# Kernel optimization log

Hardware: AMD Instinct MI355X
Metric: run time of the kernel (lower is better)

Reference implementation:

```python
import jax, jax.numpy as jnp
import numpy as np

B, N, DEG = 4, 2048, 16
HID, NH = 768, 12
D = HID // NH
N_REL = 64
E = B * N * DEG


def setup_inputs() -> dict:
    key = jax.random.key(0)
    k_x, k_r, k_q, k_k, k_v, k_e = jax.random.split(key, 6)
    node_states = jax.random.normal(k_x, (B, N, HID), dtype=jnp.float32) * 0.02
    # Deterministically unique edges: each (b, i) attends to DEG distinct tails.
    b_idx = jnp.repeat(jnp.arange(B), N * DEG)
    i_idx = jnp.tile(jnp.repeat(jnp.arange(N), DEG), B)
    offs = jnp.tile(jnp.arange(1, DEG + 1), B * N)
    t_idx = (i_idx + offs) % N
    r_idx = jax.random.randint(k_r, (E,), 0, N_REL)
    edge_indices = jnp.stack([b_idx, i_idx, t_idx, r_idx]).astype(jnp.int32)
    # Linear params (torch: y = x @ W.T + b)
    Wq = jax.random.normal(k_q, (HID, HID), dtype=jnp.float32) * 0.02
    Wk = jax.random.normal(k_k, (HID, HID), dtype=jnp.float32) * 0.02
    Wv = jax.random.normal(k_v, (HID, HID), dtype=jnp.float32) * 0.02
    bq = jnp.zeros((HID,), jnp.float32)
    bk = jnp.zeros((HID,), jnp.float32)
    bv = jnp.zeros((HID,), jnp.float32)
    rel_emb = jax.random.normal(k_e, (N_REL, HID), dtype=jnp.float32) * 0.02
    rel_emb = rel_emb.at[0].set(0.0)  # TOKEN_TO_TOKEN_RELATION_ID zeroed
    return {"node_states": node_states, "edge_indices": edge_indices,
            "Wq": Wq, "bq": bq, "Wk": Wk, "bk": bk, "Wv": Wv, "bv": bv,
            "rel_emb": rel_emb}


def reference(node_states, edge_indices, Wq, bq, Wk, bk, Wv, bv, rel_emb):
    Bv, Nv, H = node_states.shape
    Q = node_states @ Wq.T + bq
    K = node_states @ Wk.T + bk
    V = node_states @ Wv.T + bv
    b, i, t, r = edge_indices[0], edge_indices[1], edge_indices[2], edge_indices[3]
    # Translated key: K[b, tail] - relation embedding
    k_shift = (K[b, t] - rel_emb[r]).reshape(-1, NH, D)  # (E, nh, d)
    q_e = Q[b, i].reshape(-1, NH, D)                      # (E, nh, d)
    scale = jnp.sqrt(jnp.asarray(D, node_states.dtype))
    logits = jnp.einsum('ehd,ehd->eh', q_e, k_shift) / scale  # (E, nh)
    # Sparse softmax over tail dim == segment softmax per (batch, head node)
    seg = b * Nv + i
    n_seg = Bv * Nv
    m = jax.ops.segment_max(logits, seg, num_segments=n_seg)
    ex = jnp.exp(logits - m[seg])
    den = jax.ops.segment_sum(ex, seg, num_segments=n_seg)
    probs = ex / den[seg]  # (E, nh); dropout is identity in eval
    # Aggregate: out[b, i] += probs * V[b, t]
    Vt = V.reshape(Bv, Nv, NH, D)
    contrib = probs[:, :, None] * Vt[b, t]  # (E, nh, d)
    out = jax.ops.segment_sum(contrib, seg, num_segments=n_seg)
    return out.reshape(Bv, Nv, H)
```

## Files before the change

### kernel.cpp

```cpp
#include <hip/hip_runtime.h>

#define B_    4
#define N_    2048
#define HID_  768
#define NH_   12
#define E_    131072
#define M_    8192
#define NREL_ 64
#define G_    16
#define BAND_ 32
#define VP_   40
#define PP_   40

typedef unsigned short u16;
typedef unsigned int   u32;
typedef short bf16x8 __attribute__((ext_vector_type(8)));
typedef float f32x4  __attribute__((ext_vector_type(4)));

__device__ __forceinline__ u16 f2bf(float x) {
  u32 u = __float_as_uint(x);
  u += 0x7fffu + ((u >> 16) & 1u);
  return (u16)(u >> 16);
}
__device__ __forceinline__ float bflo(u32 u) { return __uint_as_float(u << 16); }
__device__ __forceinline__ float bfhi(u32 u) { return __uint_as_float(u & 0xffff0000u); }
__device__ __forceinline__ float bf1(u16 v) { return __uint_as_float(((u32)v) << 16); }

__device__ __forceinline__ void load_lds16(const u16* g, u16* l) {
  __builtin_amdgcn_global_load_lds((__attribute__((address_space(1))) void*)(g),
                                   (__attribute__((address_space(3))) void*)(l),
                                   16, 0, 0);
}

__global__ __launch_bounds__(256) void k_convert(
    const float4* __restrict__ X, const float4* __restrict__ Wq,
    const float4* __restrict__ Wk, const float4* __restrict__ Wv,
    const float4* __restrict__ rel,
    ushort4* __restrict__ Xbf, ushort4* __restrict__ Wbf, ushort4* __restrict__ Rbf) {
  const int NX4 = (M_ * HID_) / 4;
  const int NW4 = (HID_ * HID_) / 4;
  const int NR4 = (NREL_ * HID_) / 4;
  int tid = blockIdx.x * 256 + threadIdx.x;
  const float4* src; ushort4* dst; int off;
  if (tid < NX4) { src = X; dst = Xbf; off = tid; }
  else if (tid < NX4 + 3 * NW4) {
    int t2 = tid - NX4;
    int wi = t2 / NW4;
    off = t2 - wi * NW4;
    src = (wi == 0) ? Wq : (wi == 1) ? Wk : Wv;
    dst = Wbf + (size_t)wi * NW4;
  } else {
    off = tid - NX4 - 3 * NW4;
    if (off >= NR4) return;
    src = rel; dst = Rbf;
  }
  float4 v = src[off];
  ushort4 o;
  o.x = f2bf(v.x); o.y = f2bf(v.y); o.z = f2bf(v.z); o.w = f2bf(v.w);
  dst[off] = o;
}

__global__ __launch_bounds__(256, 3) void k_gemm(
    const u16* __restrict__ Xbf, const u16* __restrict__ Wbf,
    const float* __restrict__ bq, const float* __restrict__ bk, const float* __restrict__ bv,
    u16* __restrict__ Qb, u16* __restrict__ Kb, u16* __restrict__ Vb) {
  __shared__ u16 As[128 * 64];
  __shared__ u16 Bs[192 * 64];
  const int tid = threadIdx.x;
  const int w = tid >> 6, lane = tid & 63;
  const int m0 = blockIdx.x * 128;
  const int ny = blockIdx.y;
  const int widx = ny >> 2;
  const int nl0 = (ny & 3) * 192;
  const u16* Wp = Wbf + (size_t)widx * (HID_ * HID_);
  u16* Op = (widx == 0) ? Qb : (widx == 1) ? Kb : Vb;
  const float* bias = (widx == 0) ? bq : (widx == 1) ? bk : bv;

  f32x4 acc[4][6] = {};
  const int wm = w >> 1, wn = w & 1;
  const int lm = lane & 15, lg = lane >> 4;

  for (int kt = 0; kt < HID_ / 64; ++kt) {
    const int k0 = kt * 64;
    __syncthreads();
#pragma unroll
    for (int ii = 0; ii < 4; ++ii) {
      const int sb = (ii * 4 + w) * 64;
      const int s = sb + lane;
      const int m = s >> 3;
      const int g = (s & 7) ^ (m & 7);
      load_lds16(Xbf + (size_t)(m0 + m) * HID_ + k0 + g * 8, &As[sb * 8]);
    }
#pragma unroll
    for (int ii = 0; ii < 6; ++ii) {
      const int sb = (ii * 4 + w) * 64;
      const int s = sb + lane;
      const int m = s >> 3;
      const int g = (s & 7) ^ (m & 7);
      load_lds16(Wp + (size_t)(nl0 + m) * HID_ + k0 + g * 8, &Bs[sb * 8]);
    }
    __syncthreads();
#pragma unroll
    for (int kk = 0; kk < 2; ++kk) {
      bf16x8 af[4], bfr[6];
#pragma unroll
      for (int mt = 0; mt < 4; ++mt) {
        const int m = wm * 64 + mt * 16 + lm;
        const int g = (kk * 4 + lg) ^ (m & 7);
        af[mt] = *(const bf16x8*)&As[m * 64 + g * 8];
      }
#pragma unroll
      for (int nt = 0; nt < 6; ++nt) {
        const int n = wn * 96 + nt * 16 + lm;
        const int g = (kk * 4 + lg) ^ (n & 7);
        bfr[nt] = *(const bf16x8*)&Bs[n * 64 + g * 8];
      }
#pragma unroll
      for (int mt = 0; mt < 4; ++mt)
#pragma unroll
        for (int nt = 0; nt < 6; ++nt)
          acc[mt][nt] = __builtin_amdgcn_mfma_f32_16x16x32_bf16(af[mt], bfr[nt], acc[mt][nt], 0, 0, 0);
    }
  }
#pragma unroll
  for (int nt = 0; nt < 6; ++nt) {
    const int c = nl0 + wn * 96 + nt * 16 + lm;
    const float bb = bias[c];
#pragma unroll
    for (int mt = 0; mt < 4; ++mt) {
      const int rbase = m0 + wm * 64 + mt * 16 + lg * 4;
#pragma unroll
      for (int r = 0; r < 4; ++r)
        Op[(size_t)(rbase + r) * HID_ + c] = f2bf(acc[mt][nt][r] + bb);
    }
  }
}

__global__ __launch_bounds__(256) void k_qrel(
    const u16* __restrict__ Qb, const u16* __restrict__ Rbf, u16* __restrict__ QRelb) {
  const int tid = threadIdx.x, w = tid >> 6, lane = tid & 63;
  const int lm = lane & 15, quad = lane >> 4;
  const int m0 = blockIdx.x * 32 + (w & 1) * 16;
  const int h0 = (w >> 1) * 6;
#pragma unroll
  for (int hh = 0; hh < 6; ++hh) {
    const int h = h0 + hh;
    const u16* qp = Qb + (size_t)(m0 + lm) * HID_ + h * 64 + quad * 8;
    bf16x8 a0 = *(const bf16x8*)(qp);
    bf16x8 a1 = *(const bf16x8*)(qp + 32);
#pragma unroll
    for (int rt = 0; rt < 4; ++rt) {
      const u16* rp = Rbf + (size_t)(rt * 16 + lm) * HID_ + h * 64 + quad * 8;
      bf16x8 b0 = *(const bf16x8*)(rp);
      bf16x8 b1 = *(const bf16x8*)(rp + 32);
      f32x4 c = {0.f, 0.f, 0.f, 0.f};
      c = __builtin_amdgcn_mfma_f32_16x16x32_bf16(a0, b0, c, 0, 0, 0);
      c = __builtin_amdgcn_mfma_f32_16x16x32_bf16(a1, b1, c, 0, 0, 0);
#pragma unroll
      for (int r = 0; r < 4; ++r)
        QRelb[(size_t)(m0 + quad * 4 + r) * HID_ + h * 64 + rt * 16 + lm] = f2bf(c[r]);
    }
  }
}

__global__ __launch_bounds__(256, 2) void k_attn(
    const u16* __restrict__ Qb, const u16* __restrict__ Kb, const u16* __restrict__ Vb,
    const u16* __restrict__ QRelb, const int* __restrict__ eidx,
    float* __restrict__ out) {
  __shared__ __align__(16) u16 Vt[HID_ * VP_];
  __shared__ __align__(16) u16 p_bf[NH_ * 16 * PP_];
  __shared__ u16 r_s[256];
  __shared__ int t_s[256];
  __shared__ int badf;

  const int tid = threadIdx.x;
  const int w = tid >> 6, lane = tid & 63;
  const int lm = lane & 15, quad = lane >> 4;
  const int e0b = blockIdx.x * 256;
  const int b  = eidx[e0b];
  const int i0 = eidx[E_ + e0b];
  const int bN = b * N_;

  const int sV = tid & 31, pV = tid >> 5;
  const int rowV = (i0 + 1 + sV) & (N_ - 1);
  const u16* srcV = Vb + (size_t)(bN + rowV) * HID_ + pV * 96;
  uint4 vv[12];
#pragma unroll
  for (int c = 0; c < 12; ++c) vv[c] = *(const uint4*)(srcV + c * 8);

  const u16* Qrow  = Qb + (size_t)(bN + i0 + lm) * HID_ + quad * 8;
  const u16* Krow0 = Kb + (size_t)(bN + ((i0 + 1 + lm) & (N_ - 1))) * HID_ + quad * 8;
  const u16* Krow1 = Kb + (size_t)(bN + ((i0 + 17 + lm) & (N_ - 1))) * HID_ + quad * 8;
  bf16x8 qa[3][2], ka[3][4];
#pragma unroll
  for (int hh = 0; hh < 3; ++hh) {
    const int o = (w * 3 + hh) * 64;
    qa[hh][0] = *(const bf16x8*)(Qrow + o);
    qa[hh][1] = *(const bf16x8*)(Qrow + o + 32);
    ka[hh][0] = *(const bf16x8*)(Krow0 + o);
    ka[hh][1] = *(const bf16x8*)(Krow0 + o + 32);
    ka[hh][2] = *(const bf16x8*)(Krow1 + o);
    ka[hh][3] = *(const bf16x8*)(Krow1 + o + 32);
  }

  const int t_own = eidx[2 * E_ + e0b + tid];
  const int r_own = eidx[3 * E_ + e0b + tid];
  t_s[tid] = t_own;
  r_s[tid] = (u16)r_own;
  if (tid == 0) badf = 0;
  {
    u32* pz = (u32*)p_bf;
#pragma unroll
    for (int z = 0; z < NH_ * 16 * PP_ / 2 / 256; ++z) pz[z * 256 + tid] = 0;
    const int expect = (i0 + (tid >> 4) + (tid & 15) + 1) & (N_ - 1);
    if (t_own != expect) badf = 1;
  }
  __syncthreads();
  const int bad = badf;

  if (!bad) {
#pragma unroll
    for (int c = 0; c < 12; ++c) {
      uint4 v = vv[c];
      const int d0 = pV * 96 + c * 8;
      Vt[(d0 + 0) * VP_ + sV] = (u16)(v.x);
      Vt[(d0 + 1) * VP_ + sV] = (u16)(v.x >> 16);
      Vt[(d0 + 2) * VP_ + sV] = (u16)(v.y);
      Vt[(d0 + 3) * VP_ + sV] = (u16)(v.y >> 16);
      Vt[(d0 + 4) * VP_ + sV] = (u16)(v.z);
      Vt[(d0 + 5) * VP_ + sV] = (u16)(v.z >> 16);
      Vt[(d0 + 6) * VP_ + sV] = (u16)(v.w);
      Vt[(d0 + 7) * VP_ + sV] = (u16)(v.w >> 16);
    }

    int eidx4[4]; float qrelv[3][4];
#pragma unroll
    for (int r = 0; r < 4; ++r) {
      const int il = quad * 4 + r;
      eidx4[r] = il * 16 + ((lm - il) & 15);
    }
#pragma unroll
    for (int hh = 0; hh < 3; ++hh) {
      const int h = w * 3 + hh;
#pragma unroll
      for (int r = 0; r < 4; ++r) {
        const int il = quad * 4 + r;
        qrelv[hh][r] = bf1(QRelb[(size_t)(bN + i0 + il) * HID_ + h * 64 + r_s[eidx4[r]]]);
      }
    }

#pragma unroll
    for (int hh = 0; hh < 3; ++hh) {
      const int h = w * 3 + hh;
      f32x4 c0 = {0.f, 0.f, 0.f, 0.f}, c1 = {0.f, 0.f, 0.f, 0.f};
      c0 = __builtin_amdgcn_mfma_f32_16x16x32_bf16(qa[hh][0], ka[hh][0], c0, 0, 0, 0);
      c0 = __builtin_amdgcn_mfma_f32_16x16x32_bf16(qa[hh][1], ka[hh][1], c0, 0, 0, 0);
      c1 = __builtin_amdgcn_mfma_f32_16x16x32_bf16(qa[hh][0], ka[hh][2], c1, 0, 0, 0);
      c1 = __builtin_amdgcn_mfma_f32_16x16x32_bf16(qa[hh][1], ka[hh][3], c1, 0, 0, 0);
#pragma unroll
      for (int r = 0; r < 4; ++r) {
        const int il = quad * 4 + r;
        const float val = (lm >= il) ? c0[r] : c1[r];
        const float ex = __expf((val - qrelv[hh][r]) * 0.125f);
        float den = ex;
        den += __shfl_xor(den, 1);
        den += __shfl_xor(den, 2);
        den += __shfl_xor(den, 4);
        den += __shfl_xor(den, 8);
        const float p = ex * __builtin_amdgcn_rcpf(den);
        const int slot = il + ((lm - il) & 15);
        p_bf[(h * 16 + il) * PP_ + slot] = f2bf(p);
      }
    }
    __syncthreads();

#pragma unroll
    for (int hh = 0; hh < 3; ++hh) {
      const int h = w * 3 + hh;
      bf16x8 af = *(const bf16x8*)&p_bf[(h * 16 + lm) * PP_ + quad * 8];
#pragma unroll
      for (int nt = 0; nt < 4; ++nt) {
        bf16x8 bv = *(const bf16x8*)&Vt[(h * 64 + nt * 16 + lm) * VP_ + quad * 8];
        f32x4 d = {0.f, 0.f, 0.f, 0.f};
        d = __builtin_amdgcn_mfma_f32_16x16x32_bf16(af, bv, d, 0, 0, 0);
#pragma unroll
        for (int r = 0; r < 4; ++r)
          out[(size_t)(bN + i0 + quad * 4 + r) * HID_ + h * 64 + nt * 16 + lm] = d[r];
      }
    }
  } else {
    const int il = tid >> 4;
#pragma unroll
    for (int h = 0; h < NH_; ++h) {
      const u16* qp = Qb + (size_t)(bN + i0 + il) * HID_ + h * 64;
      const u16* kp = Kb + (size_t)(bN + t_own) * HID_ + h * 64;
      float s = 0.f;
      for (int d = 0; d < 64; ++d) s += bf1(qp[d]) * bf1(kp[d]);
      const float qrel = bf1(QRelb[(size_t)(bN + i0 + il) * HID_ + h * 64 + r_own]);
      const float ex = __expf((s - qrel) * 0.125f);
      float den = ex;
      den += __shfl_xor(den, 1);
      den += __shfl_xor(den, 2);
      den += __shfl_xor(den, 4);
      den += __shfl_xor(den, 8);
      p_bf[tid * NH_ + h] = f2bf(ex * __builtin_amdgcn_rcpf(den));
    }
    __syncthreads();
#pragma unroll
    for (int gsub = 0; gsub < 4; ++gsub) {
      const int il2 = w * 4 + gsub;
      float a0[8] = {0.f,0.f,0.f,0.f,0.f,0.f,0.f,0.f};
      float a1[8] = {0.f,0.f,0.f,0.f,0.f,0.f,0.f,0.f};
      for (int j2 = 0; j2 < 16; ++j2) {
        const int t2 = t_s[il2 * 16 + j2];
        const u16* Vrow = Vb + (size_t)(bN + t2) * HID_;
        uint4 v0 = *(const uint4*)(Vrow + lane * 8);
        const float p0 = bf1(p_bf[(il2 * 16 + j2) * NH_ + (lane >> 3)]);
        a0[0] += p0 * bflo(v0.x); a0[1] += p0 * bfhi(v0.x);
        a0[2] += p0 * bflo(v0.y); a0[3] += p0 * bfhi(v0.y);
        a0[4] += p0 * bflo(v0.z); a0[5] += p0 * bfhi(v0.z);
        a0[6] += p0 * bflo(v0.w); a0[7] += p0 * bfhi(v0.w);
        if (lane < 32) {
          uint4 v1 = *(const uint4*)(Vrow + 512 + lane * 8);
          const float p1 = bf1(p_bf[(il2 * 16 + j2) * NH_ + 8 + (lane >> 3)]);
          a1[0] += p1 * bflo(v1.x); a1[1] += p1 * bfhi(v1.x);
          a1[2] += p1 * bflo(v1.y); a1[3] += p1 * bfhi(v1.y);
          a1[4] += p1 * bflo(v1.z); a1[5] += p1 * bfhi(v1.z);
          a1[6] += p1 * bflo(v1.w); a1[7] += p1 * bfhi(v1.w);
        }
      }
      float* orow = out + (size_t)(bN + i0 + il2) * HID_;
      *(float4*)(orow + lane * 8)     = make_float4(a0[0], a0[1], a0[2], a0[3]);
      *(float4*)(orow + lane * 8 + 4) = make_float4(a0[4], a0[5], a0[6], a0[7]);
      if (lane < 32) {
        *(float4*)(orow + 512 + lane * 8)     = make_float4(a1[0], a1[1], a1[2], a1[3]);
        *(float4*)(orow + 512 + lane * 8 + 4) = make_float4(a1[4], a1[5], a1[6], a1[7]);
      }
    }
  }
}

extern "C" void kernel_launch(void* const* d_in, const int* in_sizes, int n_in,
                              void* d_out, int out_size, void* d_ws, size_t ws_size,
                              hipStream_t stream) {
  const float* X   = (const float*)d_in[0];
  const int*   eidx= (const int*)d_in[1];
  const float* Wq  = (const float*)d_in[2];
  const float* bq  = (const float*)d_in[3];
  const float* Wk  = (const float*)d_in[4];
  const float* bk  = (const float*)d_in[5];
  const float* Wv  = (const float*)d_in[6];
  const float* bv  = (const float*)d_in[7];
  const float* rel = (const float*)d_in[8];
  float* out = (float*)d_out;

  char* ws = (char*)d_ws;
  u16* Xbf = (u16*)(ws);
  u16* QRelb = Xbf;
  u16* Wbf = (u16*)(ws + 12582912);
  u16* Qb  = (u16*)(ws + 16121856);
  u16* Kb  = (u16*)(ws + 28704768);
  u16* Vb  = (u16*)(ws + 41287680);
  u16* Rbf = (u16*)(ws + 53870592);

  k_convert<<<7920, 256, 0, stream>>>((const float4*)X, (const float4*)Wq,
                                      (const float4*)Wk, (const float4*)Wv,
                                      (const float4*)rel,
                                      (ushort4*)Xbf, (ushort4*)Wbf, (ushort4*)Rbf);
  k_gemm<<<dim3(64, 12), 256, 0, stream>>>(Xbf, Wbf, bq, bk, bv, Qb, Kb, Vb);
  k_qrel<<<256, 256, 0, stream>>>(Qb, Rbf, QRelb);
  k_attn<<<512, 256, 0, stream>>>(Qb, Kb, Vb, QRelb, eidx, out);
}
```

Baseline: 154.8 us.

## Rewrite QKV GEMM with larger tiles and triple-buffered async LDS pipeline

Result: no change. 153.8 us (-0.6%).

```diff
diff --git a/kernel.cpp b/kernel.cpp
--- a/kernel.cpp
+++ b/kernel.cpp
@@ -60,78 +60,108 @@
   dst[off] = o;
 }
 
-__global__ __launch_bounds__(256, 3) void k_gemm(
+__global__ __launch_bounds__(512, 2) void k_gemm(
     const u16* __restrict__ Xbf, const u16* __restrict__ Wbf,
     const float* __restrict__ bq, const float* __restrict__ bk, const float* __restrict__ bv,
     u16* __restrict__ Qb, u16* __restrict__ Kb, u16* __restrict__ Vb) {
-  __shared__ u16 As[128 * 64];
-  __shared__ u16 Bs[192 * 64];
+  extern __shared__ __align__(16) u16 lds[];
   const int tid = threadIdx.x;
   const int w = tid >> 6, lane = tid & 63;
-  const int m0 = blockIdx.x * 128;
-  const int ny = blockIdx.y;
-  const int widx = ny >> 2;
-  const int nl0 = (ny & 3) * 192;
-  const u16* Wp = Wbf + (size_t)widx * (HID_ * HID_);
-  u16* Op = (widx == 0) ? Qb : (widx == 1) ? Kb : Vb;
-  const float* bias = (widx == 0) ? bq : (widx == 1) ? bk : bv;
-
-  f32x4 acc[4][6] = {};
+  const int lm = lane & 15, lg = lane >> 4;
   const int wm = w >> 1, wn = w & 1;
-  const int lm = lane & 15, lg = lane >> 4;
-
-  for (int kt = 0; kt < HID_ / 64; ++kt) {
-    const int k0 = kt * 64;
-    __syncthreads();
-#pragma unroll
-    for (int ii = 0; ii < 4; ++ii) {
-      const int sb = (ii * 4 + w) * 64;
-      const int s = sb + lane;
-      const int m = s >> 3;
-      const int g = (s & 7) ^ (m & 7);
-      load_lds16(Xbf + (size_t)(m0 + m) * HID_ + k0 + g * 8, &As[sb * 8]);
-    }
-#pragma unroll
-    for (int ii = 0; ii < 6; ++ii) {
-      const int sb = (ii * 4 + w) * 64;
-      const int s = sb + lane;
-      const int m = s >> 3;
-      const int g = (s & 7) ^ (m & 7);
-      load_lds16(Wp + (size_t)(nl0 + m) * HID_ + k0 + g * 8, &Bs[sb * 8]);
-    }
-    __syncthreads();
-#pragma unroll
-    for (int kk = 0; kk < 2; ++kk) {
-      bf16x8 af[4], bfr[6];
-#pragma unroll
-      for (int mt = 0; mt < 4; ++mt) {
-        const int m = wm * 64 + mt * 16 + lm;
-        const int g = (kk * 4 + lg) ^ (m & 7);
-        af[mt] = *(const bf16x8*)&As[m * 64 + g * 8];
-      }
-#pragma unroll
-      for (int nt = 0; nt < 6; ++nt) {
-        const int n = wn * 96 + nt * 16 + lm;
-        const int g = (kk * 4 + lg) ^ (n & 7);
-        bfr[nt] = *(const bf16x8*)&Bs[n * 64 + g * 8];
-      }
-#pragma unroll
-      for (int mt = 0; mt < 4; ++mt)
-#pragma unroll
-        for (int nt = 0; nt < 6; ++nt)
-          acc[mt][nt] = __builtin_amdgcn_mfma_f32_16x16x32_bf16(af[mt], bfr[nt], acc[mt][nt], 0, 0, 0);
-    }
-  }
-#pragma unroll
-  for (int nt = 0; nt < 6; ++nt) {
-    const int c = nl0 + wn * 96 + nt * 16 + lm;
-    const float bb = bias[c];
+  const int m0  = blockIdx.x * 256;
+  const int n0g = blockIdx.y * 288;
+
+  f32x4 acc[4][9] = {};
+
+  auto STAGE = [&](int bi, int kt) {
+    const int k0 = kt * 32;
+    u16* Ab = lds + bi * (256 * 32);
+    u16* Bb = lds + 3 * (256 * 32) + bi * (288 * 32);
+#pragma unroll
+    for (int ii = 0; ii < 2; ++ii) {
+      const int sb = (ii * 8 + w) * 64;
+      const int s  = sb + lane;
+      const int m  = s >> 2;
+      const int g  = (s & 3) ^ ((m >> 1) & 3);
+      load_lds16(Xbf + (size_t)(m0 + m) * HID_ + k0 + g * 8, Ab + sb * 8);
+    }
+#pragma unroll
+    for (int ii = 0; ii < 2; ++ii) {
+      const int sb = (ii * 8 + w) * 64;
+      const int s  = sb + lane;
+      const int m  = s >> 2;
+      const int g  = (s & 3) ^ ((m >> 1) & 3);
+      load_lds16(Wbf + (size_t)(n0g + m) * HID_ + k0 + g * 8, Bb + sb * 8);
+    }
+    if (w < 2) {
+      const int sb = (16 + w) * 64;
+      const int s  = sb + lane;
+      const int m  = s >> 2;
+      const int g  = (s & 3) ^ ((m >> 1) & 3);
+      load_lds16(Wbf + (size_t)(n0g + m) * HID_ + k0 + g * 8, Bb + sb * 8);
+    }
+  };
+
+  auto COMPUTE = [&](int bi) {
+    const u16* As = lds + bi * (256 * 32);
+    const u16* Bs = lds + 3 * (256 * 32) + bi * (288 * 32);
+    bf16x8 bfv[9];
+#pragma unroll
+    for (int nt = 0; nt < 9; ++nt) {
+      const int n = wn * 144 + nt * 16 + lm;
+      const int g = lg ^ ((n >> 1) & 3);
+      bfv[nt] = *(const bf16x8*)&Bs[n * 32 + g * 8];
+    }
+    __builtin_amdgcn_s_setprio(1);
+#pragma unroll
+    for (int mt = 0; mt < 4; ++mt) {
+      const int m = wm * 64 + mt * 16 + lm;
+      const int g = lg ^ ((m >> 1) & 3);
+      bf16x8 af = *(const bf16x8*)&As[m * 32 + g * 8];
+#pragma unroll
+      for (int nt = 0; nt < 9; ++nt)
+        acc[mt][nt] = __builtin_amdgcn_mfma_f32_16x16x32_bf16(af, bfv[nt], acc[mt][nt], 0, 0, 0);
+    }
+    __builtin_amdgcn_s_setprio(0);
+  };
+
+#define BODYK(KT, BC, BS, DOSTAGE, VMZ)                                  \
+  do {                                                                   \
+    if (VMZ)        asm volatile("s_waitcnt vmcnt(0)" ::: "memory");     \
+    else if (w < 2) asm volatile("s_waitcnt vmcnt(5)" ::: "memory");     \
+    else            asm volatile("s_waitcnt vmcnt(4)" ::: "memory");     \
+    __builtin_amdgcn_s_barrier();                                        \
+    asm volatile("" ::: "memory");                                       \
+    if (DOSTAGE) STAGE(BS, (KT) + 2);                                    \
+    COMPUTE(BC);                                                         \
+  } while (0)
+
+  STAGE(0, 0);
+  STAGE(1, 1);
+  for (int t3 = 0; t3 < 21; t3 += 3) {
+    BODYK(t3 + 0, 0, 2, true, false);
+    BODYK(t3 + 1, 1, 0, true, false);
+    BODYK(t3 + 2, 2, 1, true, false);
+  }
+  BODYK(21, 0, 2, true,  false);
+  BODYK(22, 1, 0, false, false);
+  BODYK(23, 2, 1, false, true);
+#undef BODYK
+
+#pragma unroll
+  for (int nt = 0; nt < 9; ++nt) {
+    const int c    = n0g + wn * 144 + nt * 16 + lm;
+    const int widx = (c >= 1536) ? 2 : (c >= 768) ? 1 : 0;
+    const int col  = c - widx * 768;
+    const float bb = ((widx == 0) ? bq : (widx == 1) ? bk : bv)[col];
+    u16* Op = (widx == 0) ? Qb : (widx == 1) ? Kb : Vb;
 #pragma unroll
     for (int mt = 0; mt < 4; ++mt) {
       const int rbase = m0 + wm * 64 + mt * 16 + lg * 4;
 #pragma unroll
       for (int r = 0; r < 4; ++r)
-        Op[(size_t)(rbase + r) * HID_ + c] = f2bf(acc[mt][nt][r] + bb);
+        Op[(size_t)(rbase + r) * HID_ + col] = f2bf(acc[mt][nt][r] + bb);
     }
   }
 }
@@ -363,11 +393,18 @@
   u16* Vb  = (u16*)(ws + 41287680);
   u16* Rbf = (u16*)(ws + 53870592);
 
+  static bool s_attr = false;
+  if (!s_attr) {
+    (void)hipFuncSetAttribute((const void*)k_gemm,
+                              hipFuncAttributeMaxDynamicSharedMemorySize, 104448);
+    s_attr = true;
+  }
+
   k_convert<<<7920, 256, 0, stream>>>((const float4*)X, (const float4*)Wq,
                                       (const float4*)Wk, (const float4*)Wv,
                                       (const float4*)rel,
                                       (ushort4*)Xbf, (ushort4*)Wbf, (ushort4*)Rbf);
-  k_gemm<<<dim3(64, 12), 256, 0, stream>>>(Xbf, Wbf, bq, bk, bv, Qb, Kb, Vb);
+  k_gemm<<<dim3(32, 8), 512, 104448, stream>>>(Xbf, Wbf, bq, bk, bv, Qb, Kb, Vb);
   k_qrel<<<256, 256, 0, stream>>>(Qb, Rbf, QRelb);
   k_attn<<<512, 256, 0, stream>>>(Qb, Kb, Vb, QRelb, eidx, out);
 }
```

## Restructure QKV GEMM: stage full-K A tile in LDS, stream weights from global

Applied to the files above, without the earlier changes.

New measurement: 182.5 us. 1.18x slower.

```diff
diff --git a/kernel.cpp b/kernel.cpp
--- a/kernel.cpp
+++ b/kernel.cpp
@@ -60,78 +60,70 @@
   dst[off] = o;
 }
 
-__global__ __launch_bounds__(256, 3) void k_gemm(
+__global__ __launch_bounds__(512, 2) void k_gemm(
     const u16* __restrict__ Xbf, const u16* __restrict__ Wbf,
     const float* __restrict__ bq, const float* __restrict__ bk, const float* __restrict__ bv,
     u16* __restrict__ Qb, u16* __restrict__ Kb, u16* __restrict__ Vb) {
-  __shared__ u16 As[128 * 64];
-  __shared__ u16 Bs[192 * 64];
+  extern __shared__ __align__(16) u16 Alds[];
   const int tid = threadIdx.x;
   const int w = tid >> 6, lane = tid & 63;
-  const int m0 = blockIdx.x * 128;
-  const int ny = blockIdx.y;
-  const int widx = ny >> 2;
-  const int nl0 = (ny & 3) * 192;
-  const u16* Wp = Wbf + (size_t)widx * (HID_ * HID_);
-  u16* Op = (widx == 0) ? Qb : (widx == 1) ? Kb : Vb;
-  const float* bias = (widx == 0) ? bq : (widx == 1) ? bk : bv;
-
-  f32x4 acc[4][6] = {};
-  const int wm = w >> 1, wn = w & 1;
   const int lm = lane & 15, lg = lane >> 4;
-
-  for (int kt = 0; kt < HID_ / 64; ++kt) {
-    const int k0 = kt * 64;
-    __syncthreads();
-#pragma unroll
-    for (int ii = 0; ii < 4; ++ii) {
-      const int sb = (ii * 4 + w) * 64;
-      const int s = sb + lane;
-      const int m = s >> 3;
-      const int g = (s & 7) ^ (m & 7);
-      load_lds16(Xbf + (size_t)(m0 + m) * HID_ + k0 + g * 8, &As[sb * 8]);
-    }
-#pragma unroll
-    for (int ii = 0; ii < 6; ++ii) {
-      const int sb = (ii * 4 + w) * 64;
-      const int s = sb + lane;
-      const int m = s >> 3;
-      const int g = (s & 7) ^ (m & 7);
-      load_lds16(Wp + (size_t)(nl0 + m) * HID_ + k0 + g * 8, &Bs[sb * 8]);
-    }
-    __syncthreads();
-#pragma unroll
-    for (int kk = 0; kk < 2; ++kk) {
-      bf16x8 af[4], bfr[6];
-#pragma unroll
-      for (int mt = 0; mt < 4; ++mt) {
-        const int m = wm * 64 + mt * 16 + lm;
-        const int g = (kk * 4 + lg) ^ (m & 7);
-        af[mt] = *(const bf16x8*)&As[m * 64 + g * 8];
-      }
-#pragma unroll
-      for (int nt = 0; nt < 6; ++nt) {
-        const int n = wn * 96 + nt * 16 + lm;
-        const int g = (kk * 4 + lg) ^ (n & 7);
-        bfr[nt] = *(const bf16x8*)&Bs[n * 64 + g * 8];
-      }
-#pragma unroll
-      for (int mt = 0; mt < 4; ++mt)
-#pragma unroll
-        for (int nt = 0; nt < 6; ++nt)
-          acc[mt][nt] = __builtin_amdgcn_mfma_f32_16x16x32_bf16(af[mt], bfr[nt], acc[mt][nt], 0, 0, 0);
-    }
-  }
-#pragma unroll
-  for (int nt = 0; nt < 6; ++nt) {
-    const int c = nl0 + wn * 96 + nt * 16 + lm;
-    const float bb = bias[c];
+  const int m0   = blockIdx.x * 64;
+  const int colb = blockIdx.y * 1152 + w * 144;
+
+#pragma unroll
+  for (int ii = 0; ii < 12; ++ii) {
+    const int d  = ii * 512 + tid;
+    const int kt = d >> 8;
+    const int m  = (d >> 2) & 63;
+    const int q  = (d & 3) ^ ((m >> 1) & 3);
+    load_lds16(Xbf + (size_t)(m0 + m) * HID_ + kt * 32 + q * 8, Alds + (size_t)d * 8);
+  }
+  __syncthreads();
+
+  const u16* Abase = Alds + lm * 32 + (lg ^ ((lm >> 1) & 3)) * 8;
+  const u16* wp = Wbf + (size_t)(colb + lm) * HID_ + lg * 8;
+
+  f32x4 acc[4][9] = {};
+  bf16x8 a0[4], a1[4], b0[9], b1[9];
+
+#define LOADA(DST, KT) { _Pragma("unroll") for (int mt = 0; mt < 4; ++mt)        \
+    DST[mt] = *(const bf16x8*)(Abase + (KT) * 2048 + mt * 512); }
+#define LOADB(DST, KT) { _Pragma("unroll") for (int nt = 0; nt < 9; ++nt)        \
+    DST[nt] = *(const bf16x8*)(wp + (size_t)nt * (16 * HID_) + (KT) * 32); }
+#define MM(AA, BB) { _Pragma("unroll") for (int mt = 0; mt < 4; ++mt)            \
+    _Pragma("unroll") for (int nt = 0; nt < 9; ++nt)                             \
+      acc[mt][nt] = __builtin_amdgcn_mfma_f32_16x16x32_bf16(AA[mt], BB[nt], acc[mt][nt], 0, 0, 0); }
+
+  LOADA(a0, 0); LOADB(b0, 0);
+  for (int i = 0; i < 11; ++i) {
+    const int k1 = 2 * i + 1;
+    LOADA(a1, k1); LOADB(b1, k1);
+    MM(a0, b0);
+    LOADA(a0, k1 + 1); LOADB(b0, k1 + 1);
+    MM(a1, b1);
+  }
+  LOADA(a1, 23); LOADB(b1, 23);
+  MM(a0, b0);
+  MM(a1, b1);
+
+#undef MM
+#undef LOADB
+#undef LOADA
+
+#pragma unroll
+  for (int nt = 0; nt < 9; ++nt) {
+    const int c    = colb + nt * 16 + lm;
+    const int widx = (c >= 1536) ? 2 : (c >= 768) ? 1 : 0;
+    const int col  = c - widx * 768;
+    const float bb = ((widx == 0) ? bq : (widx == 1) ? bk : bv)[col];
+    u16* Op = (widx == 0) ? Qb : (widx == 1) ? Kb : Vb;
 #pragma unroll
     for (int mt = 0; mt < 4; ++mt) {
-      const int rbase = m0 + wm * 64 + mt * 16 + lg * 4;
+      const int rbase = m0 + mt * 16 + lg * 4;
 #pragma unroll
       for (int r = 0; r < 4; ++r)
-        Op[(size_t)(rbase + r) * HID_ + c] = f2bf(acc[mt][nt][r] + bb);
+        Op[(size_t)(rbase + r) * HID_ + col] = f2bf(acc[mt][nt][r] + bb);
     }
   }
 }
@@ -363,11 +355,18 @@
   u16* Vb  = (u16*)(ws + 41287680);
   u16* Rbf = (u16*)(ws + 53870592);
 
+  static bool s_attr = false;
+  if (!s_attr) {
+    (void)hipFuncSetAttribute((const void*)k_gemm,
+                              hipFuncAttributeMaxDynamicSharedMemorySize, 98304);
+    s_attr = true;
+  }
+
   k_convert<<<7920, 256, 0, stream>>>((const float4*)X, (const float4*)Wq,
                                       (const float4*)Wk, (const float4*)Wv,
                                       (const float4*)rel,
                                       (ushort4*)Xbf, (ushort4*)Wbf, (ushort4*)Rbf);
-  k_gemm<<<dim3(64, 12), 256, 0, stream>>>(Xbf, Wbf, bq, bk, bv, Qb, Kb, Vb);
+  k_gemm<<<dim3(128, 2), 512, 98304, stream>>>(Xbf, Wbf, bq, bk, bv, Qb, Kb, Vb);
   k_qrel<<<256, 256, 0, stream>>>(Qb, Rbf, QRelb);
   k_attn<<<512, 256, 0, stream>>>(Qb, Kb, Vb, QRelb, eidx, out);
 }
```
